# Optimization experiments

Hardware: AMD Instinct MI355X
Metric: run time of the kernel (lower is better)

The kernel has to match this reference:

```python
import jax, jax.numpy as jnp
import numpy as np

N_HEADS = 16
HEAD_DIM = 128


def _rotate_half(x):
    x1, x2 = jnp.split(x, 2, axis=-1)
    return jnp.concatenate((-x2, x1), axis=-1)


def setup_inputs() -> dict:
    key = jax.random.key(0)
    ks = jax.random.split(key, 6)
    B, T, D = 2, 2048, 2048
    d = D // N_HEADS  # 128
    x = jax.random.normal(ks[0], (B, T, D), dtype=jnp.float32)
    # RoPE tables (shape [1,1,T,head_dim]) built as in standard implementations
    inv_freq = 1.0 / (10000.0 ** (jnp.arange(0, d, 2, dtype=jnp.float32) / d))
    ang = jnp.arange(T, dtype=jnp.float32)[:, None] * inv_freq[None, :]  # [T, d/2]
    emb = jnp.concatenate((ang, ang), axis=-1)  # [T, d]
    rope_cos = jnp.cos(emb)[None, None]
    rope_sin = jnp.sin(emb)[None, None]
    qkv_w = jax.random.normal(ks[1], (3 * D, D), dtype=jnp.float32) * (1.0 / np.sqrt(D))
    qkv_b = jnp.zeros((3 * D,), dtype=jnp.float32)
    out_w = jax.random.normal(ks[2], (D, D), dtype=jnp.float32) * (1.0 / np.sqrt(D))
    out_b = jnp.zeros((D,), dtype=jnp.float32)
    return {"x": x, "rope_cos": rope_cos, "rope_sin": rope_sin,
            "qkv_w": qkv_w, "qkv_b": qkv_b, "out_w": out_w, "out_b": out_b}


def reference(x, rope_cos, rope_sin, qkv_w, qkv_b, out_w, out_b):
    B, T, D = x.shape
    H, d = N_HEADS, D // N_HEADS
    # fused QKV projection: [B,T,3D] -> [3,B,H,T,d]
    qkv = (jnp.einsum('btd,ed->bte', x, qkv_w) + qkv_b)
    qkv = qkv.reshape(B, T, 3, H, d).transpose(2, 0, 3, 1, 4)
    q, k, v = qkv[0], qkv[1], qkv[2]
    cos = rope_cos[:, :, :T, :].astype(q.dtype)
    sin = rope_sin[:, :, :T, :].astype(q.dtype)
    q = q * cos + _rotate_half(q) * sin
    k = k * cos + _rotate_half(k) * sin
    # causal SDPA
    scale = 1.0 / jnp.sqrt(jnp.array(d, dtype=q.dtype))
    scores = jnp.einsum('bhqd,bhkd->bhqk', q, k) * scale  # [B,H,T,T]
    causal = jnp.tril(jnp.ones((T, T), dtype=bool))
    scores = jnp.where(causal, scores, jnp.finfo(scores.dtype).min)
    attn = jax.nn.softmax(scores, axis=-1)
    out = jnp.einsum('bhqk,bhkd->bhqd', attn, v)  # [B,H,T,d]
    out = out.transpose(0, 2, 1, 3).reshape(B, T, D)
    return jnp.einsum('btd,ed->bte', out, out_w) + out_b
```

## Files before the change

kernel.cpp:

```cpp
#include <hip/hip_runtime.h>
#include <cstdint>
#include <cstddef>

typedef unsigned short u16;
using bf16x8 = __attribute__((ext_vector_type(8))) short;
using f32x4  = __attribute__((ext_vector_type(4))) float;

#define MFMA16(a, b, c) __builtin_amdgcn_mfma_f32_16x16x32_bf16((a), (b), (c), 0, 0, 0)

__device__ __forceinline__ u16 f2bf(float f) {
  union { float f; unsigned u; } x; x.f = f;
  unsigned r = x.u + 0x7fffu + ((x.u >> 16) & 1u);
  return (u16)(r >> 16);
}
__device__ __forceinline__ float bf2f(u16 h) {
  union { unsigned u; float f; } x; x.u = ((unsigned)h) << 16;
  return x.f;
}
__device__ __forceinline__ void gll16(const void* g, void* l) {
  __builtin_amdgcn_global_load_lds((const __attribute__((address_space(1))) void*)g,
                                   (__attribute__((address_space(3))) void*)l, 16, 0, 0);
}

union U8 { bf16x8 v; u16 u[8]; };

__global__ __launch_bounds__(256) void cvt_kernel(const float* __restrict__ in,
                                                  u16* __restrict__ out, int n4) {
  int i = blockIdx.x * blockDim.x + threadIdx.x;
  if (i >= n4) return;
  float4 v = ((const float4*)in)[i];
  ushort4 o;
  o.x = f2bf(v.x); o.y = f2bf(v.y); o.z = f2bf(v.z); o.w = f2bf(v.w);
  ((ushort4*)out)[i] = o;
}

__global__ __launch_bounds__(512, 2) void gemm_bt256(const u16* __restrict__ A,
                                                     const u16* __restrict__ Bw,
                                                     const float* __restrict__ bias,
                                                     void* __restrict__ Cout,
                                                     int M, int N, int K, int out_bf16) {
  __shared__ u16 As[3][8192];
  __shared__ u16 Bs[3][8192];
  const int tid = threadIdx.x;
  const int lane = tid & 63, wave = tid >> 6;
  const int col = lane & 15, quad = lane >> 4;
  const int wr = wave >> 2, wc = wave & 3;
  const int bm = blockIdx.y, bn = blockIdx.x;
  const u16* Ag = A + (size_t)bm * 256 * K;
  const u16* Bg = Bw + (size_t)bn * 256 * K;
  const int r0 = tid >> 2, r1 = (tid + 512) >> 2;
  const int sl = tid & 3;
  const size_t off0 = (size_t)r0 * K + ((sl ^ ((r0 >> 1) & 3)) << 3);
  const size_t off1 = (size_t)r1 * K + ((sl ^ ((r1 >> 1) & 3)) << 3);
  f32x4 acc[8][4] = {};
  const int NT = K >> 5;

#define STAGE_A(buf, k0) do { \
    gll16(Ag + off0 + (k0), (void*)(As[buf] + tid * 8)); \
    gll16(Ag + off1 + (k0), (void*)(As[buf] + 4096 + tid * 8)); } while (0)
#define STAGE_B(buf, k0) do { \
    gll16(Bg + off0 + (k0), (void*)(Bs[buf] + tid * 8)); \
    gll16(Bg + off1 + (k0), (void*)(Bs[buf] + 4096 + tid * 8)); } while (0)

  STAGE_A(0, 0); STAGE_B(0, 0);
  if (NT > 1) {
    STAGE_A(1, 32); STAGE_B(1, 32);
    asm volatile("s_waitcnt vmcnt(4)" ::: "memory");
  } else {
    asm volatile("s_waitcnt vmcnt(0)" ::: "memory");
  }
  __builtin_amdgcn_s_barrier();

  int cur = 0;
  for (int t = 0; t < NT; ++t) {
    const u16* Ab = As[cur];
    const u16* Bb = Bs[cur];
    int nx2 = cur + 2; if (nx2 >= 3) nx2 -= 3;
    const bool pf = (t + 2) < NT;
    const int k2 = (t + 2) << 5;
    bf16x8 af[4], bfr[4];
#pragma unroll
    for (int i = 0; i < 4; i++) {
      const int row = wr * 128 + i * 16 + col;
      af[i] = *(const bf16x8*)&Ab[row * 32 + ((quad ^ ((row >> 1) & 3)) << 3)];
    }
#pragma unroll
    for (int j = 0; j < 4; j++) {
      const int row = wc * 64 + j * 16 + col;
      bfr[j] = *(const bf16x8*)&Bb[row * 32 + ((quad ^ ((row >> 1) & 3)) << 3)];
    }
    if (pf) STAGE_A(nx2, k2);
    __builtin_amdgcn_s_barrier();
    __builtin_amdgcn_s_setprio(1);
#pragma unroll
    for (int i = 0; i < 4; i++)
#pragma unroll
      for (int j = 0; j < 4; j++)
        acc[i][j] = MFMA16(af[i], bfr[j], acc[i][j]);
    __builtin_amdgcn_s_setprio(0);
    __builtin_amdgcn_s_barrier();
#pragma unroll
    for (int i = 0; i < 4; i++) {
      const int row = wr * 128 + (i + 4) * 16 + col;
      af[i] = *(const bf16x8*)&Ab[row * 32 + ((quad ^ ((row >> 1) & 3)) << 3)];
    }
    if (pf) STAGE_B(nx2, k2);
    __builtin_amdgcn_s_barrier();
    __builtin_amdgcn_s_setprio(1);
#pragma unroll
    for (int i = 0; i < 4; i++)
#pragma unroll
      for (int j = 0; j < 4; j++)
        acc[4 + i][j] = MFMA16(af[i], bfr[j], acc[4 + i][j]);
    __builtin_amdgcn_s_setprio(0);
    if (pf) asm volatile("s_waitcnt vmcnt(4)" ::: "memory");
    else    asm volatile("s_waitcnt vmcnt(0)" ::: "memory");
    __builtin_amdgcn_s_barrier();
    cur = (cur + 1 == 3) ? 0 : cur + 1;
  }

#pragma unroll
  for (int i = 0; i < 8; i++) {
    const int row0 = bm * 256 + wr * 128 + i * 16 + quad * 4;
#pragma unroll
    for (int j = 0; j < 4; j++) {
      const int cn = bn * 256 + wc * 64 + j * 16 + col;
      const float bv = bias[cn];
#pragma unroll
      for (int r = 0; r < 4; r++) {
        float v = acc[i][j][r] + bv;
        size_t off = (size_t)(row0 + r) * N + cn;
        if (out_bf16) ((u16*)Cout)[off] = f2bf(v);
        else          ((float*)Cout)[off] = v;
      }
    }
  }
#undef STAGE_A
#undef STAGE_B
}

__global__ __launch_bounds__(256) void rope_kernel(const u16* __restrict__ qkv,
                                                   const float* __restrict__ cosT,
                                                   const float* __restrict__ sinT,
                                                   u16* __restrict__ qo,
                                                   u16* __restrict__ ko,
                                                   u16* __restrict__ vt) {
  __shared__ u16 vs[128 * 72];
  const int bh = blockIdx.x;
  const int b = bh >> 4, h = bh & 15;
  const int tb = blockIdx.y;
  const int tid = threadIdx.x;
  const int tl = tid >> 2;
  const int g = tid & 3;
  const int t = tb * 64 + tl;
  const size_t qrow = ((size_t)(b * 2048 + t)) * 6144 + h * 128;
  const size_t orow = ((size_t)bh * 2048 + t) * 128;
  const int tt = t * 128;
  const int dl = g * 16, dh = 64 + dl;
  const float scale = 0.08838834764831845f;
#pragma unroll
  for (int cch = 0; cch < 2; cch++) {
    const int o8 = cch * 8;
    U8 ql, qh, kl, kh, vl, vh;
    ql.v = *(const bf16x8*)&qkv[qrow + dl + o8];
    qh.v = *(const bf16x8*)&qkv[qrow + dh + o8];
    kl.v = *(const bf16x8*)&qkv[qrow + 2048 + dl + o8];
    kh.v = *(const bf16x8*)&qkv[qrow + 2048 + dh + o8];
    vl.v = *(const bf16x8*)&qkv[qrow + 4096 + dl + o8];
    vh.v = *(const bf16x8*)&qkv[qrow + 4096 + dh + o8];
    float cl[8], ch_[8], sl[8], sh_[8];
    *(float4*)&cl[0]  = *(const float4*)&cosT[tt + dl + o8];
    *(float4*)&cl[4]  = *(const float4*)&cosT[tt + dl + o8 + 4];
    *(float4*)&ch_[0] = *(const float4*)&cosT[tt + dh + o8];
    *(float4*)&ch_[4] = *(const float4*)&cosT[tt + dh + o8 + 4];
    *(float4*)&sl[0]  = *(const float4*)&sinT[tt + dl + o8];
    *(float4*)&sl[4]  = *(const float4*)&sinT[tt + dl + o8 + 4];
    *(float4*)&sh_[0] = *(const float4*)&sinT[tt + dh + o8];
    *(float4*)&sh_[4] = *(const float4*)&sinT[tt + dh + o8 + 4];
    U8 aq, bq, ak, bk;
#pragma unroll
    for (int i = 0; i < 8; i++) {
      float qlf = bf2f(ql.u[i]), qhf = bf2f(qh.u[i]);
      float klf = bf2f(kl.u[i]), khf = bf2f(kh.u[i]);
      aq.u[i] = f2bf((qlf * cl[i]  - qhf * sl[i])  * scale);
      bq.u[i] = f2bf((qhf * ch_[i] + qlf * sh_[i]) * scale);
      ak.u[i] = f2bf(klf * cl[i]  - khf * sl[i]);
      bk.u[i] = f2bf(khf * ch_[i] + klf * sh_[i]);
    }
    *(bf16x8*)&qo[orow + dl + o8] = aq.v;
    *(bf16x8*)&qo[orow + dh + o8] = bq.v;
    *(bf16x8*)&ko[orow + dl + o8] = ak.v;
    *(bf16x8*)&ko[orow + dh + o8] = bk.v;
#pragma unroll
    for (int i = 0; i < 8; i++) {
      vs[(dl + o8 + i) * 72 + tl] = vl.u[i];
      vs[(dh + o8 + i) * 72 + tl] = vh.u[i];
    }
  }
  __syncthreads();
#pragma unroll
  for (int c = 0; c < 4; c++) {
    int idx = c * 256 + tid;
    int dd = idx >> 3, chk = idx & 7;
    bf16x8 vv = *(const bf16x8*)&vs[dd * 72 + chk * 8];
    *(bf16x8*)&vt[((size_t)bh * 128 + dd) * 2048 + tb * 64 + chk * 8] = vv;
  }
}

__global__ __launch_bounds__(256) void attn_kernel(const u16* __restrict__ Q,
                                                   const u16* __restrict__ Kk,
                                                   const u16* __restrict__ Vt,
                                                   u16* __restrict__ O) {
  __shared__ u16 Ks[64 * 136];
  __shared__ u16 Vs[128 * 72];
  __shared__ u16 Ps[4][16 * 72];
  const int bh = blockIdx.y, b = bh >> 4, h = bh & 15;
  const int qtile = gridDim.x - 1 - blockIdx.x;
  const int qb = qtile * 128;
  const int tid = threadIdx.x, wave = tid >> 6, lane = tid & 63;
  const int col = lane & 15, quad = lane >> 4;
  const int qw0 = qb + wave * 32;
  const int qw1 = qw0 + 16;
  const u16* Qg = Q + (size_t)bh * 2048 * 128;
  const u16* Kg = Kk + (size_t)bh * 2048 * 128;
  const u16* Vg = Vt + (size_t)bh * 128 * 2048;
  bf16x8 qf0[4], qf1[4];
#pragma unroll
  for (int c = 0; c < 4; c++) {
    qf0[c] = *(const bf16x8*)&Qg[(size_t)(qw0 + col) * 128 + c * 32 + quad * 8];
    qf1[c] = *(const bf16x8*)&Qg[(size_t)(qw1 + col) * 128 + c * 32 + quad * 8];
  }
  f32x4 o0[8] = {}, o1[8] = {};
  float ls0[4] = {0.f, 0.f, 0.f, 0.f}, ls1[4] = {0.f, 0.f, 0.f, 0.f};
  const int ntiles = (qb + 128) >> 6;
  const int kr = tid >> 2, kc = (tid & 3) * 8;
  const int vr = tid >> 1, vc = (tid & 1) * 8;
  for (int it = 0; it < ntiles; ++it) {
    const int kt = it << 6;
    __syncthreads();
#pragma unroll
    for (int u = 0; u < 4; u++)
      *(bf16x8*)&Ks[kr * 136 + kc + u * 32] =
          *(const bf16x8*)&Kg[(size_t)(kt + kr) * 128 + kc + u * 32];
#pragma unroll
    for (int u = 0; u < 4; u++)
      *(bf16x8*)&Vs[vr * 72 + vc + u * 16] =
          *(const bf16x8*)&Vg[(size_t)vr * 2048 + kt + vc + u * 16];
    __syncthreads();
    if (kt > qw1 + 15) continue;
    const bool do0 = (kt <= qw0 + 15);
    f32x4 s0[4] = {}, s1[4] = {};
#pragma unroll
    for (int c = 0; c < 4; c++) {
#pragma unroll
      for (int kg = 0; kg < 4; kg++) {
        bf16x8 kf = *(const bf16x8*)&Ks[(kg * 16 + col) * 136 + c * 32 + quad * 8];
        s0[kg] = MFMA16(qf0[c], kf, s0[kg]);
        s1[kg] = MFMA16(qf1[c], kf, s1[kg]);
      }
    }
    u16* pw = Ps[wave];
    if (do0) {
#pragma unroll
      for (int kg = 0; kg < 4; kg++)
#pragma unroll
        for (int r = 0; r < 4; r++) {
          int key = kt + kg * 16 + col, qg = qw0 + quad * 4 + r;
          float p = (key <= qg) ? __expf(s0[kg][r]) : 0.f;
          ls0[r] += p;
          pw[(quad * 4 + r) * 72 + kg * 16 + col] = f2bf(p);
        }
#pragma unroll
      for (int ks = 0; ks < 64; ks += 32) {
        bf16x8 pf = *(const bf16x8*)&pw[col * 72 + ks + quad * 8];
#pragma unroll
        for (int dt = 0; dt < 8; dt++) {
          bf16x8 vf = *(const bf16x8*)&Vs[(dt * 16 + col) * 72 + ks + quad * 8];
          o0[dt] = MFMA16(pf, vf, o0[dt]);
        }
      }
    }
    {
#pragma unroll
      for (int kg = 0; kg < 4; kg++)
#pragma unroll
        for (int r = 0; r < 4; r++) {
          int key = kt + kg * 16 + col, qg = qw1 + quad * 4 + r;
          float p = (key <= qg) ? __expf(s1[kg][r]) : 0.f;
          ls1[r] += p;
          pw[(quad * 4 + r) * 72 + kg * 16 + col] = f2bf(p);
        }
#pragma unroll
      for (int ks = 0; ks < 64; ks += 32) {
        bf16x8 pf = *(const bf16x8*)&pw[col * 72 + ks + quad * 8];
#pragma unroll
        for (int dt = 0; dt < 8; dt++) {
          bf16x8 vf = *(const bf16x8*)&Vs[(dt * 16 + col) * 72 + ks + quad * 8];
          o1[dt] = MFMA16(pf, vf, o1[dt]);
        }
      }
    }
  }
#pragma unroll
  for (int st = 1; st < 16; st <<= 1)
#pragma unroll
    for (int r = 0; r < 4; r++) {
      ls0[r] += __shfl_xor(ls0[r], st);
      ls1[r] += __shfl_xor(ls1[r], st);
    }
#pragma unroll
  for (int r = 0; r < 4; r++) {
    float inv0 = 1.0f / ls0[r], inv1 = 1.0f / ls1[r];
    size_t row0 = ((size_t)(b * 2048 + qw0 + quad * 4 + r)) * 2048 + h * 128;
    size_t row1 = ((size_t)(b * 2048 + qw1 + quad * 4 + r)) * 2048 + h * 128;
#pragma unroll
    for (int dt = 0; dt < 8; dt++) {
      O[row0 + dt * 16 + col] = f2bf(o0[dt][r] * inv0);
      O[row1 + dt * 16 + col] = f2bf(o1[dt][r] * inv1);
    }
  }
}

extern "C" void kernel_launch(void* const* d_in, const int* in_sizes, int n_in,
                              void* d_out, int out_size, void* d_ws, size_t ws_size,
                              hipStream_t stream) {
  const float* x        = (const float*)d_in[0];
  const float* rope_cos = (const float*)d_in[1];
  const float* rope_sin = (const float*)d_in[2];
  const float* qkv_w    = (const float*)d_in[3];
  const float* qkv_b    = (const float*)d_in[4];
  const float* out_w    = (const float*)d_in[5];
  const float* out_b    = (const float*)d_in[6];
  float* out = (float*)d_out;
  u16* ws = (u16*)d_ws;
  u16* xb    = ws;
  u16* wqkvb = xb + 8388608;
  u16* woutb = wqkvb + 12582912;
  u16* qkvb  = woutb + 4194304;
  u16* qb    = qkvb + 25165824;
  u16* kb    = qb + 8388608;
  u16* vtb   = kb + 8388608;
  u16* attnb = xb;

  cvt_kernel<<<8192, 256, 0, stream>>>(x, xb, 2097152);
  cvt_kernel<<<12288, 256, 0, stream>>>(qkv_w, wqkvb, 3145728);
  cvt_kernel<<<4096, 256, 0, stream>>>(out_w, woutb, 1048576);
  gemm_bt256<<<dim3(24, 16), 512, 0, stream>>>(xb, wqkvb, qkv_b, qkvb, 4096, 6144, 2048, 1);
  rope_kernel<<<dim3(32, 32), 256, 0, stream>>>(qkvb, rope_cos, rope_sin, qb, kb, vtb);
  attn_kernel<<<dim3(16, 32), 256, 0, stream>>>(qb, kb, vtb, attnb);
  gemm_bt256<<<dim3(8, 16), 512, 0, stream>>>(attnb, woutb, out_b, out, 4096, 2048, 2048, 0);
}
```

Baseline: 473.0 us.

## Template GEMM on N-tile width and register-prefetch K/V tiles in attention

```diff
diff --git a/kernel.cpp b/kernel.cpp
--- a/kernel.cpp
+++ b/kernel.cpp
@@ -34,97 +34,91 @@
   ((ushort4*)out)[i] = o;
 }
 
-__global__ __launch_bounds__(512, 2) void gemm_bt256(const u16* __restrict__ A,
-                                                     const u16* __restrict__ Bw,
-                                                     const float* __restrict__ bias,
-                                                     void* __restrict__ Cout,
-                                                     int M, int N, int K, int out_bf16) {
+template<int NBF>
+__global__ __launch_bounds__(512, 2) void gemm_nt(const u16* __restrict__ A,
+                                                  const u16* __restrict__ Bw,
+                                                  const float* __restrict__ bias,
+                                                  void* __restrict__ Cout,
+                                                  int M, int N, int K, int out_bf16) {
   __shared__ u16 As[3][8192];
-  __shared__ u16 Bs[3][8192];
+  __shared__ u16 Bs[3][NBF * 2048];
   const int tid = threadIdx.x;
   const int lane = tid & 63, wave = tid >> 6;
   const int col = lane & 15, quad = lane >> 4;
   const int wr = wave >> 2, wc = wave & 3;
   const int bm = blockIdx.y, bn = blockIdx.x;
   const u16* Ag = A + (size_t)bm * 256 * K;
-  const u16* Bg = Bw + (size_t)bn * 256 * K;
-  const int r0 = tid >> 2, r1 = (tid + 512) >> 2;
-  const int sl = tid & 3;
-  const size_t off0 = (size_t)r0 * K + ((sl ^ ((r0 >> 1) & 3)) << 3);
-  const size_t off1 = (size_t)r1 * K + ((sl ^ ((r1 >> 1) & 3)) << 3);
-  f32x4 acc[8][4] = {};
+  const u16* Bg = Bw + (size_t)bn * (NBF * 64) * K;
+  const int srow = tid >> 2;
+  const int ssw = ((tid & 3) ^ ((srow >> 1) & 3)) << 3;
+  const size_t ga0 = (size_t)srow * K + ssw;
+  const size_t ga1 = (size_t)(srow + 128) * K + ssw;
+  const int swq = (quad ^ ((col >> 1) & 3)) << 3;
+  const int aro = (wr * 128 + col) * 32 + swq;
+  const int bro = (wc * (NBF * 16) + col) * 32 + swq;
+  f32x4 acc[8][NBF] = {};
   const int NT = K >> 5;
 
-#define STAGE_A(buf, k0) do { \
-    gll16(Ag + off0 + (k0), (void*)(As[buf] + tid * 8)); \
-    gll16(Ag + off1 + (k0), (void*)(As[buf] + 4096 + tid * 8)); } while (0)
-#define STAGE_B(buf, k0) do { \
-    gll16(Bg + off0 + (k0), (void*)(Bs[buf] + tid * 8)); \
-    gll16(Bg + off1 + (k0), (void*)(Bs[buf] + 4096 + tid * 8)); } while (0)
-
-  STAGE_A(0, 0); STAGE_B(0, 0);
-  if (NT > 1) {
-    STAGE_A(1, 32); STAGE_B(1, 32);
-    asm volatile("s_waitcnt vmcnt(4)" ::: "memory");
-  } else {
-    asm volatile("s_waitcnt vmcnt(0)" ::: "memory");
-  }
+#define STG_A(BI, KT) do { \
+    gll16(Ag + ga0 + (KT), (void*)(&As[BI][0] + tid * 8)); \
+    gll16(Ag + ga1 + (KT), (void*)(&As[BI][0] + 4096 + tid * 8)); } while (0)
+#define STG_B(BI, KT) do { \
+    gll16(Bg + ga0 + (KT), (void*)(&Bs[BI][0] + tid * 8)); \
+    if (NBF == 4) gll16(Bg + ga1 + (KT), (void*)(&Bs[BI][0] + 4096 + tid * 8)); } while (0)
+
+  STG_A(0, 0); STG_B(0, 0); STG_A(1, 32); STG_B(1, 32);
+  if (NBF == 4) asm volatile("s_waitcnt vmcnt(4)" ::: "memory");
+  else          asm volatile("s_waitcnt vmcnt(3)" ::: "memory");
   __builtin_amdgcn_s_barrier();
 
-  int cur = 0;
+  int cA = 0, cB = 1, cC = 2;
   for (int t = 0; t < NT; ++t) {
-    const u16* Ab = As[cur];
-    const u16* Bb = Bs[cur];
-    int nx2 = cur + 2; if (nx2 >= 3) nx2 -= 3;
+    const u16* Ab = &As[cA][0];
+    const u16* Bb = &Bs[cA][0];
     const bool pf = (t + 2) < NT;
     const int k2 = (t + 2) << 5;
-    bf16x8 af[4], bfr[4];
-#pragma unroll
-    for (int i = 0; i < 4; i++) {
-      const int row = wr * 128 + i * 16 + col;
-      af[i] = *(const bf16x8*)&Ab[row * 32 + ((quad ^ ((row >> 1) & 3)) << 3)];
-    }
-#pragma unroll
-    for (int j = 0; j < 4; j++) {
-      const int row = wc * 64 + j * 16 + col;
-      bfr[j] = *(const bf16x8*)&Bb[row * 32 + ((quad ^ ((row >> 1) & 3)) << 3)];
-    }
-    if (pf) STAGE_A(nx2, k2);
+    bf16x8 a1[4], a2[4], b[NBF];
+#pragma unroll
+    for (int j = 0; j < 4; j++) a1[j] = *(const bf16x8*)&Ab[aro + j * 512];
+#pragma unroll
+    for (int n = 0; n < NBF; n++) b[n] = *(const bf16x8*)&Bb[bro + n * 512];
+    if (pf) STG_A(cC, k2);
     __builtin_amdgcn_s_barrier();
     __builtin_amdgcn_s_setprio(1);
 #pragma unroll
-    for (int i = 0; i < 4; i++)
-#pragma unroll
-      for (int j = 0; j < 4; j++)
-        acc[i][j] = MFMA16(af[i], bfr[j], acc[i][j]);
+    for (int m = 0; m < 4; m++)
+#pragma unroll
+      for (int n = 0; n < NBF; n++)
+        acc[m][n] = MFMA16(a1[m], b[n], acc[m][n]);
     __builtin_amdgcn_s_setprio(0);
     __builtin_amdgcn_s_barrier();
 #pragma unroll
-    for (int i = 0; i < 4; i++) {
-      const int row = wr * 128 + (i + 4) * 16 + col;
-      af[i] = *(const bf16x8*)&Ab[row * 32 + ((quad ^ ((row >> 1) & 3)) << 3)];
-    }
-    if (pf) STAGE_B(nx2, k2);
+    for (int j = 0; j < 4; j++) a2[j] = *(const bf16x8*)&Ab[aro + (4 + j) * 512];
+    if (pf) STG_B(cC, k2);
     __builtin_amdgcn_s_barrier();
     __builtin_amdgcn_s_setprio(1);
 #pragma unroll
-    for (int i = 0; i < 4; i++)
-#pragma unroll
-      for (int j = 0; j < 4; j++)
-        acc[4 + i][j] = MFMA16(af[i], bfr[j], acc[4 + i][j]);
+    for (int m = 0; m < 4; m++)
+#pragma unroll
+      for (int n = 0; n < NBF; n++)
+        acc[4 + m][n] = MFMA16(a2[m], b[n], acc[4 + m][n]);
     __builtin_amdgcn_s_setprio(0);
-    if (pf) asm volatile("s_waitcnt vmcnt(4)" ::: "memory");
-    else    asm volatile("s_waitcnt vmcnt(0)" ::: "memory");
+    if (pf) {
+      if (NBF == 4) asm volatile("s_waitcnt vmcnt(4)" ::: "memory");
+      else          asm volatile("s_waitcnt vmcnt(3)" ::: "memory");
+    } else {
+      asm volatile("s_waitcnt vmcnt(0)" ::: "memory");
+    }
     __builtin_amdgcn_s_barrier();
-    cur = (cur + 1 == 3) ? 0 : cur + 1;
+    int tmp = cA; cA = cB; cB = cC; cC = tmp;
   }
 
 #pragma unroll
   for (int i = 0; i < 8; i++) {
     const int row0 = bm * 256 + wr * 128 + i * 16 + quad * 4;
 #pragma unroll
-    for (int j = 0; j < 4; j++) {
-      const int cn = bn * 256 + wc * 64 + j * 16 + col;
+    for (int j = 0; j < NBF; j++) {
+      const int cn = bn * (NBF * 64) + wc * (NBF * 16) + j * 16 + col;
       const float bv = bias[cn];
 #pragma unroll
       for (int r = 0; r < 4; r++) {
@@ -135,8 +129,8 @@
       }
     }
   }
-#undef STAGE_A
-#undef STAGE_B
+#undef STG_A
+#undef STG_B
 }
 
 __global__ __launch_bounds__(256) void rope_kernel(const u16* __restrict__ qkv,
@@ -235,18 +229,30 @@
   const int ntiles = (qb + 128) >> 6;
   const int kr = tid >> 2, kc = (tid & 3) * 8;
   const int vr = tid >> 1, vc = (tid & 1) * 8;
+  bf16x8 kreg[4], vreg[4];
+#pragma unroll
+  for (int u = 0; u < 4; u++) {
+    kreg[u] = *(const bf16x8*)&Kg[(size_t)kr * 128 + kc + u * 32];
+    vreg[u] = *(const bf16x8*)&Vg[(size_t)vr * 2048 + vc + u * 16];
+  }
   for (int it = 0; it < ntiles; ++it) {
     const int kt = it << 6;
     __syncthreads();
 #pragma unroll
     for (int u = 0; u < 4; u++)
-      *(bf16x8*)&Ks[kr * 136 + kc + u * 32] =
-          *(const bf16x8*)&Kg[(size_t)(kt + kr) * 128 + kc + u * 32];
+      *(bf16x8*)&Ks[kr * 136 + kc + u * 32] = kreg[u];
 #pragma unroll
     for (int u = 0; u < 4; u++)
-      *(bf16x8*)&Vs[vr * 72 + vc + u * 16] =
-          *(const bf16x8*)&Vg[(size_t)vr * 2048 + kt + vc + u * 16];
+      *(bf16x8*)&Vs[vr * 72 + vc + u * 16] = vreg[u];
     __syncthreads();
+    if (it + 1 < ntiles) {
+      const int kt2 = kt + 64;
+#pragma unroll
+      for (int u = 0; u < 4; u++) {
+        kreg[u] = *(const bf16x8*)&Kg[(size_t)(kt2 + kr) * 128 + kc + u * 32];
+        vreg[u] = *(const bf16x8*)&Vg[(size_t)vr * 2048 + kt2 + vc + u * 16];
+      }
+    }
     if (kt > qw1 + 15) continue;
     const bool do0 = (kt <= qw0 + 15);
     f32x4 s0[4] = {}, s1[4] = {};
@@ -345,8 +351,8 @@
   cvt_kernel<<<8192, 256, 0, stream>>>(x, xb, 2097152);
   cvt_kernel<<<12288, 256, 0, stream>>>(qkv_w, wqkvb, 3145728);
   cvt_kernel<<<4096, 256, 0, stream>>>(out_w, woutb, 1048576);
-  gemm_bt256<<<dim3(24, 16), 512, 0, stream>>>(xb, wqkvb, qkv_b, qkvb, 4096, 6144, 2048, 1);
+  gemm_nt<4><<<dim3(24, 16), 512, 0, stream>>>(xb, wqkvb, qkv_b, qkvb, 4096, 6144, 2048, 1);
   rope_kernel<<<dim3(32, 32), 256, 0, stream>>>(qkvb, rope_cos, rope_sin, qb, kb, vtb);
   attn_kernel<<<dim3(16, 32), 256, 0, stream>>>(qb, kb, vtb, attnb);
-  gemm_bt256<<<dim3(8, 16), 512, 0, stream>>>(attnb, woutb, out_b, out, 4096, 2048, 2048, 0);
-}
+  gemm_nt<2><<<dim3(16, 16), 512, 0, stream>>>(attnb, woutb, out_b, out, 4096, 2048, 2048, 0);
+}
```

Result: slower. 518.4 us (+9.6%).
